# Performance work log

Measured on AMD Instinct MI355X. Metric: run time of the kernel, lower is better.

The kernel has to match this reference:

```python
import jax, jax.numpy as jnp
import numpy as np

N_NODES = 100000


def _gcn_layer(x, src, dst, W, b, num_nodes):
    # Linear transform first (PyG GCNConv applies Linear before propagate).
    h = x @ W.T  # [N, out]
    # Degree (with self loops already included in src/dst), computed on target.
    ones = jnp.ones(dst.shape[0], dtype=h.dtype)
    deg = jax.ops.segment_sum(ones, dst, num_segments=num_nodes)
    dinv = jnp.where(deg > 0, jax.lax.rsqrt(deg), 0.0)
    norm = dinv[src] * dinv[dst]  # [E]
    msg = h[src] * norm[:, None]  # gather + per-edge scale, [E, out]
    out = jax.ops.segment_sum(msg, dst, num_segments=num_nodes)
    return out + b


def setup_inputs() -> dict:
    key = jax.random.key(0)
    k1, k2, k3, k4, k5, k6 = jax.random.split(key, 6)
    d = 64
    x = jax.random.normal(k1, (N_NODES, d), dtype=jnp.float32)
    edge_index = jax.random.randint(k2, (2, 1600000), 0, N_NODES, dtype=jnp.int64)
    s = 1.0 / np.sqrt(d)
    W1 = jax.random.normal(k3, (d, d), dtype=jnp.float32) * s
    b1 = jax.random.normal(k4, (d,), dtype=jnp.float32) * 0.01
    W2 = jax.random.normal(k5, (d, d), dtype=jnp.float32) * s
    b2 = jax.random.normal(k6, (d,), dtype=jnp.float32) * 0.01
    return {"x": x, "edge_index": edge_index, "W1": W1, "b1": b1, "W2": W2, "b2": b2}


def reference(x, edge_index, W1, b1, W2, b2):
    n = x.shape[0]
    loop = jnp.arange(n, dtype=edge_index.dtype)
    src = jnp.concatenate([edge_index[0], loop])  # add self loops
    dst = jnp.concatenate([edge_index[1], loop])
    h = _gcn_layer(x, src, dst, W1, b1, n)
    out = _gcn_layer(h, src, dst, W2, b2, n)
    return out
```

## Files before the change

kernel.cpp:

```cpp
#include <hip/hip_runtime.h>
#include <hip/hip_fp16.h>


#define D 64
#define NPB 128
#define MAXB 784
#define CHUNK 8192

__global__ __launch_bounds__(256) void hist_kernel(const int* __restrict__ dst,
                                                   int* __restrict__ counts,
                                                   int nE, int B) {
    __shared__ int hist[MAXB];
    int c = blockIdx.x;
    for (int b = threadIdx.x; b < B; b += 256) hist[b] = 0;
    __syncthreads();
    int e0 = c * CHUNK;
#pragma unroll
    for (int i = 0; i < CHUNK / 256; ++i) {
        int e = e0 + i * 256 + threadIdx.x;
        if (e < nE) atomicAdd(&hist[dst[e] >> 7], 1);
    }
    __syncthreads();
    for (int b = threadIdx.x; b < B; b += 256) counts[c * B + b] = hist[b];
}

__global__ __launch_bounds__(256) void scan_chunks(const int* __restrict__ counts,
                                                   int* __restrict__ base,
                                                   int* __restrict__ bucketTotal,
                                                   int B, int C) {
    int b = blockIdx.x * 4 + (threadIdx.x >> 6);
    if (b >= B) return;
    int lane = threadIdx.x & 63;
    int running = 0;
    for (int c0 = 0; c0 < C; c0 += 64) {
        int c = c0 + lane;
        int v = (c < C) ? counts[c * B + b] : 0;
        int x = v;
#pragma unroll
        for (int s = 1; s < 64; s <<= 1) {
            int u = __shfl_up(x, s);
            if (lane >= s) x += u;
        }
        if (c < C) base[c * B + b] = running + x - v;
        running += __shfl(x, 63);
    }
    if (lane == 0) bucketTotal[b] = running;
}

__global__ __launch_bounds__(1024) void scan_buckets(const int* __restrict__ bucketTotal,
                                                     int* __restrict__ bucketBase, int B) {
    __shared__ int sdata[1024];
    int t = threadIdx.x;
    int v = (t < B) ? bucketTotal[t] : 0;
    sdata[t] = v;
    __syncthreads();
    for (int s = 1; s < 1024; s <<= 1) {
        int u = (t >= s) ? sdata[t - s] : 0;
        __syncthreads();
        sdata[t] += u;
        __syncthreads();
    }
    if (t < B) bucketBase[t] = sdata[t] - v;
    if (t == B - 1) bucketBase[B] = sdata[t];
}

__global__ __launch_bounds__(256) void scatter0_kernel(const int* __restrict__ src,
                                                       const int* __restrict__ dst,
                                                       const int* __restrict__ base,
                                                       const int* __restrict__ bbase,
                                                       int* __restrict__ entries0,
                                                       int nE, int B) {
    __shared__ int cur[MAXB];
    int c = blockIdx.x;
    for (int b = threadIdx.x; b < B; b += 256) cur[b] = base[c * B + b] + bbase[b];
    __syncthreads();
    int e0 = c * CHUNK;
#pragma unroll
    for (int i = 0; i < CHUNK / 256; ++i) {
        int e = e0 + i * 256 + threadIdx.x;
        if (e < nE) {
            int s = src[e], d = dst[e];
            int pos = atomicAdd(&cur[d >> 7], 1);
            entries0[pos] = s | ((d & (NPB - 1)) << 17);
        }
    }
}

__global__ __launch_bounds__(256) void regroup_count(const int* __restrict__ entries0,
                                                     const int* __restrict__ bbase,
                                                     int* __restrict__ off,
                                                     int* __restrict__ deg,
                                                     float* __restrict__ dinv, int N) {
    __shared__ int cnt[NPB];
    __shared__ int scn[NPB];
    int b = blockIdx.x;
    int t = threadIdx.x;
    if (t < NPB) cnt[t] = 0;
    __syncthreads();
    int s0 = bbase[b], s1 = bbase[b + 1];
    for (int p = s0 + t; p < s1; p += 256)
        atomicAdd(&cnt[(entries0[p] >> 17) & (NPB - 1)], 1);
    __syncthreads();
    if (t < NPB) scn[t] = cnt[t];
    __syncthreads();
    for (int s = 1; s < NPB; s <<= 1) {
        int u = 0;
        if (t < NPB && t >= s) u = scn[t - s];
        __syncthreads();
        if (t < NPB) scn[t] += u;
        __syncthreads();
    }
    if (t < NPB) {
        int node = b * NPB + t;
        if (node < N) {
            int c = cnt[t];
            off[node]  = s0 + scn[t] - c;
            deg[node]  = c;
            dinv[node] = rsqrtf((float)c + 1.0f);
        }
    }
}

__global__ __launch_bounds__(256) void regroup_scatter(const int* __restrict__ entries0,
                                                       const int* __restrict__ bbase,
                                                       const int* __restrict__ off,
                                                       const float* __restrict__ dinv,
                                                       int2* __restrict__ entries1, int N) {
    __shared__ int cur[NPB];
    int b = blockIdx.x;
    int t = threadIdx.x;
    if (t < NPB) {
        int node = b * NPB + t;
        cur[t] = (node < N) ? off[node] : 0;
    }
    __syncthreads();
    int s0 = bbase[b], s1 = bbase[b + 1];
    for (int p = s0 + t; p < s1; p += 256) {
        int e = entries0[p];
        int s = e & 0x1FFFF;
        int dloc = (e >> 17) & (NPB - 1);
        int pos = atomicAdd(&cur[dloc], 1);
        float nrm = dinv[s] * dinv[b * NPB + dloc];
        entries1[pos] = make_int2(s, __float_as_int(nrm));
    }
}

__global__ __launch_bounds__(256) void aggregate2(const int2* __restrict__ csr,
                                                  const int* __restrict__ off,
                                                  const int* __restrict__ deg,
                                                  const float* __restrict__ dinv,
                                                  const __half* __restrict__ H,
                                                  const float* __restrict__ bias,
                                                  float* __restrict__ out, int N) {
    int node = blockIdx.x * 4 + (threadIdx.x >> 6);
    if (node >= N) return;
    int lane = threadIdx.x & 63;
    int p2 = lane & 31;
    int h  = lane >> 5;
    const __half2* H2 = (const __half2*)H;
    float2 acc = make_float2(0.0f, 0.0f);
    int beg = off[node];
    int end = beg + deg[node];
    int p = beg;
    for (; p + 8 <= end; p += 8) {
        int2 e0 = csr[p + 0 + h];
        int2 e1 = csr[p + 2 + h];
        int2 e2 = csr[p + 4 + h];
        int2 e3 = csr[p + 6 + h];
        __half2 g0 = H2[(size_t)e0.x * 32 + p2];
        __half2 g1 = H2[(size_t)e1.x * 32 + p2];
        __half2 g2 = H2[(size_t)e2.x * 32 + p2];
        __half2 g3 = H2[(size_t)e3.x * 32 + p2];
        float c0 = __int_as_float(e0.y), c1 = __int_as_float(e1.y);
        float c2 = __int_as_float(e2.y), c3 = __int_as_float(e3.y);
        float2 f0 = __half22float2(g0), f1 = __half22float2(g1);
        float2 f2 = __half22float2(g2), f3 = __half22float2(g3);
        acc.x += f0.x * c0; acc.y += f0.y * c0;
        acc.x += f1.x * c1; acc.y += f1.y * c1;
        acc.x += f2.x * c2; acc.y += f2.y * c2;
        acc.x += f3.x * c3; acc.y += f3.y * c3;
    }
    for (; p + 2 <= end; p += 2) {
        int2 e0 = csr[p + h];
        __half2 g0 = H2[(size_t)e0.x * 32 + p2];
        float c0 = __int_as_float(e0.y);
        float2 f0 = __half22float2(g0);
        acc.x += f0.x * c0; acc.y += f0.y * c0;
    }
    if (p < end && h == 0) {
        int2 e0 = csr[p];
        __half2 g0 = H2[(size_t)e0.x * 32 + p2];
        float c0 = __int_as_float(e0.y);
        float2 f0 = __half22float2(g0);
        acc.x += f0.x * c0; acc.y += f0.y * c0;
    }
    acc.x += __shfl_xor(acc.x, 32);
    acc.y += __shfl_xor(acc.y, 32);
    if (h == 0) {
        float dd = dinv[node];
        float s = dd * dd;
        float2 hs = __half22float2(H2[(size_t)node * 32 + p2]);
        float2 bv = ((const float2*)bias)[p2];
        float2 o;
        o.x = acc.x + bv.x + hs.x * s;
        o.y = acc.y + bv.y + hs.y * s;
        ((float2*)(out + (size_t)node * D))[p2] = o;
    }
}

__global__ __launch_bounds__(256) void gemm_xwt_h(const float* __restrict__ X,
                                                  const float* __restrict__ W,
                                                  __half* __restrict__ H, int N) {
    __shared__ float xt[64 * 68];
    __shared__ float wt[64 * 68];
    const int t = threadIdx.x;
    const int i0 = blockIdx.x * 64;
#pragma unroll
    for (int r = 0; r < 16; ++r) {
        int idx = r * 256 + t;
        int j = idx >> 6, k = idx & 63;
        wt[k * 68 + j] = W[idx];
    }
#pragma unroll
    for (int r = 0; r < 16; ++r) {
        int idx = r * 256 + t;
        int i = idx >> 6, k = idx & 63;
        float v = 0.0f;
        if (i0 + i < N) v = X[(size_t)(i0 + i) * D + k];
        xt[k * 68 + i] = v;
    }
    __syncthreads();
    const int tn = (t & 15) * 4;
    const int tc = (t >> 4) * 4;
    float acc[4][4] = {};
#pragma unroll 8
    for (int k = 0; k < 64; ++k) {
        const float4 xa = *(const float4*)(xt + k * 68 + tn);
        const float4 wb = *(const float4*)(wt + k * 68 + tc);
        acc[0][0] += xa.x * wb.x; acc[0][1] += xa.x * wb.y; acc[0][2] += xa.x * wb.z; acc[0][3] += xa.x * wb.w;
        acc[1][0] += xa.y * wb.x; acc[1][1] += xa.y * wb.y; acc[1][2] += xa.y * wb.z; acc[1][3] += xa.y * wb.w;
        acc[2][0] += xa.z * wb.x; acc[2][1] += xa.z * wb.y; acc[2][2] += xa.z * wb.z; acc[2][3] += xa.z * wb.w;
        acc[3][0] += xa.w * wb.x; acc[3][1] += xa.w * wb.y; acc[3][2] += xa.w * wb.z; acc[3][3] += xa.w * wb.w;
    }
#pragma unroll
    for (int a = 0; a < 4; ++a) {
        int i = i0 + tn + a;
        if (i < N) {
            union { __half2 h2[2]; uint2 u2; } pk;
            pk.h2[0].x = __float2half_rn(acc[a][0]);
            pk.h2[0].y = __float2half_rn(acc[a][1]);
            pk.h2[1].x = __float2half_rn(acc[a][2]);
            pk.h2[1].y = __float2half_rn(acc[a][3]);
            *(uint2*)(&H[(size_t)i * D + tc]) = pk.u2;
        }
    }
}

__global__ __launch_bounds__(256) void deg_kernel(const int* __restrict__ dst,
                                                  int* __restrict__ deg, int nE) {
    int e = blockIdx.x * 256 + threadIdx.x;
    if (e < nE) atomicAdd(&deg[dst[e]], 1);
}

__global__ __launch_bounds__(256) void dinv_kernel(const int* __restrict__ deg,
                                                   float* __restrict__ dinv, int N) {
    int i = blockIdx.x * 256 + threadIdx.x;
    if (i < N) dinv[i] = rsqrtf((float)deg[i] + 1.0f);
}

__global__ __launch_bounds__(256) void gemm_xwt(const float* __restrict__ X,
                                                const float* __restrict__ W,
                                                float* __restrict__ H, int N) {
    __shared__ float xt[64 * 68];
    __shared__ float wt[64 * 68];
    const int t = threadIdx.x;
    const int i0 = blockIdx.x * 64;
#pragma unroll
    for (int r = 0; r < 16; ++r) {
        int idx = r * 256 + t;
        int j = idx >> 6, k = idx & 63;
        wt[k * 68 + j] = W[idx];
    }
#pragma unroll
    for (int r = 0; r < 16; ++r) {
        int idx = r * 256 + t;
        int i = idx >> 6, k = idx & 63;
        float v = 0.0f;
        if (i0 + i < N) v = X[(size_t)(i0 + i) * D + k];
        xt[k * 68 + i] = v;
    }
    __syncthreads();
    const int tn = (t & 15) * 4;
    const int tc = (t >> 4) * 4;
    float acc[4][4] = {};
#pragma unroll 8
    for (int k = 0; k < 64; ++k) {
        const float4 xa = *(const float4*)(xt + k * 68 + tn);
        const float4 wb = *(const float4*)(wt + k * 68 + tc);
        acc[0][0] += xa.x * wb.x; acc[0][1] += xa.x * wb.y; acc[0][2] += xa.x * wb.z; acc[0][3] += xa.x * wb.w;
        acc[1][0] += xa.y * wb.x; acc[1][1] += xa.y * wb.y; acc[1][2] += xa.y * wb.z; acc[1][3] += xa.y * wb.w;
        acc[2][0] += xa.z * wb.x; acc[2][1] += xa.z * wb.y; acc[2][2] += xa.z * wb.z; acc[2][3] += xa.z * wb.w;
        acc[3][0] += xa.w * wb.x; acc[3][1] += xa.w * wb.y; acc[3][2] += xa.w * wb.z; acc[3][3] += xa.w * wb.w;
    }
#pragma unroll
    for (int a = 0; a < 4; ++a) {
        int i = i0 + tn + a;
        if (i < N) {
            float4 o = make_float4(acc[a][0], acc[a][1], acc[a][2], acc[a][3]);
            *(float4*)(H + (size_t)i * D + tc) = o;
        }
    }
}

__global__ __launch_bounds__(256) void init_out(const float* __restrict__ H,
                                                const float* __restrict__ dinv,
                                                const float* __restrict__ b,
                                                float* __restrict__ out, int N) {
    int idx4 = blockIdx.x * 256 + threadIdx.x;
    if (idx4 >= N * 16) return;
    int i = idx4 >> 4;
    int jc = idx4 & 15;
    float di = dinv[i];
    float s = di * di;
    float4 h4 = ((const float4*)H)[idx4];
    float4 b4 = ((const float4*)b)[jc];
    ((float4*)out)[idx4] = make_float4(b4.x + h4.x * s, b4.y + h4.y * s,
                                       b4.z + h4.z * s, b4.w + h4.w * s);
}

__global__ __launch_bounds__(256) void edge_scatter(const int* __restrict__ src,
                                                    const int* __restrict__ dst,
                                                    const float* __restrict__ dinv,
                                                    const float* __restrict__ H,
                                                    float* __restrict__ out, int nE) {
    int tid = blockIdx.x * 256 + threadIdx.x;
    int e = tid >> 4;
    if (e >= nE) return;
    int l = tid & 15;
    int s = src[e];
    int d = dst[e];
    float c = dinv[s] * dinv[d];
    float4 v = ((const float4*)H)[s * 16 + l];
    float* o = out + (size_t)d * D + l * 4;
    unsafeAtomicAdd(o + 0, v.x * c);
    unsafeAtomicAdd(o + 1, v.y * c);
    unsafeAtomicAdd(o + 2, v.z * c);
    unsafeAtomicAdd(o + 3, v.w * c);
}

static inline size_t align_up(size_t v, size_t a) { return (v + a - 1) & ~(a - 1); }

extern "C" void kernel_launch(void* const* d_in, const int* in_sizes, int n_in,
                              void* d_out, int out_size, void* d_ws, size_t ws_size,
                              hipStream_t stream) {
    const float* x  = (const float*)d_in[0];
    const int*   ei = (const int*)d_in[1];
    const float* W1 = (const float*)d_in[2];
    const float* b1 = (const float*)d_in[3];
    const float* W2 = (const float*)d_in[4];
    const float* b2 = (const float*)d_in[5];
    float* out = (float*)d_out;

    const int N  = in_sizes[0] / D;
    const int nE = in_sizes[1] / 2;
    const int* src = ei;
    const int* dstv = ei + nE;

    const int B = (N + NPB - 1) / NPB;
    const int C = (nE + CHUNK - 1) / CHUNK;

    char* base_p = (char*)d_ws;
    size_t o = 0;
    int* counts = (int*)(base_p + o);  o = align_up(o + (size_t)C * B * 4, 256);
    int* cbase  = (int*)(base_p + o);  o = align_up(o + (size_t)C * B * 4, 256);
    int* btot   = (int*)(base_p + o);  o = align_up(o + (size_t)B * 4, 256);
    int* bbase  = (int*)(base_p + o);  o = align_up(o + (size_t)(B + 1) * 4, 256);
    int* off    = (int*)(base_p + o);  o = align_up(o + (size_t)N * 4, 256);
    int* deg    = (int*)(base_p + o);  o = align_up(o + (size_t)N * 4, 256);
    float* dinv = (float*)(base_p + o); o = align_up(o + (size_t)N * 4, 256);
    int2* entries1 = (int2*)(base_p + o); o = align_up(o + (size_t)nE * 8, 256);
    size_t r2 = (size_t)nE * 4 > (size_t)N * D * 2 ? (size_t)nE * 4 : (size_t)N * D * 2;
    int* entries0 = (int*)(base_p + o);
    __half* Hh    = (__half*)(base_p + o);
    o = align_up(o + r2, 256);
    size_t need = o;

    int gb_n = (N + 255) / 256;
    int gb_g = (N + 63) / 64;
    int gb_e = (nE + 255) / 256;

    if (ws_size >= need && B <= MAXB && B <= 1024) {
        hist_kernel<<<C, 256, 0, stream>>>(dstv, counts, nE, B);
        scan_chunks<<<(B + 3) / 4, 256, 0, stream>>>(counts, cbase, btot, B, C);
        scan_buckets<<<1, 1024, 0, stream>>>(btot, bbase, B);
        scatter0_kernel<<<C, 256, 0, stream>>>(src, dstv, cbase, bbase, entries0, nE, B);
        regroup_count<<<B, 256, 0, stream>>>(entries0, bbase, off, deg, dinv, N);
        regroup_scatter<<<B, 256, 0, stream>>>(entries0, bbase, off, dinv, entries1, N);

        int gb_a = (N + 3) / 4;
        gemm_xwt_h<<<gb_g, 256, 0, stream>>>(x, W1, Hh, N);
        aggregate2<<<gb_a, 256, 0, stream>>>(entries1, off, deg, dinv, Hh, b1, out, N);
        gemm_xwt_h<<<gb_g, 256, 0, stream>>>(out, W2, Hh, N);
        aggregate2<<<gb_a, 256, 0, stream>>>(entries1, off, deg, dinv, Hh, b2, out, N);
    } else {
        size_t fo = 0;
        int* fdeg    = (int*)(base_p + fo);  fo = align_up(fo + (size_t)N * 4, 256);
        float* fdinv = (float*)(base_p + fo); fo = align_up(fo + (size_t)N * 4, 256);
        float* bufA  = (float*)(base_p + fo);
        hipMemsetAsync(fdeg, 0, (size_t)N * 4, stream);
        deg_kernel<<<gb_e, 256, 0, stream>>>(dstv, fdeg, nE);
        dinv_kernel<<<gb_n, 256, 0, stream>>>(fdeg, fdinv, N);
        int gb_i = (N * 16 + 255) / 256;
        int gb_e16 = (int)(((long long)nE * 16 + 255) / 256);
        gemm_xwt<<<gb_g, 256, 0, stream>>>(x, W1, bufA, N);
        init_out<<<gb_i, 256, 0, stream>>>(bufA, fdinv, b1, out, N);
        edge_scatter<<<gb_e16, 256, 0, stream>>>(src, dstv, fdinv, bufA, out, nE);
        gemm_xwt<<<gb_g, 256, 0, stream>>>(out, W2, bufA, N);
        init_out<<<gb_i, 256, 0, stream>>>(bufA, fdinv, b2, out, N);
        edge_scatter<<<gb_e16, 256, 0, stream>>>(src, dstv, fdinv, bufA, out, nE);
    }
}
```

Measured before the change: 298.3 us.

## Fuse CSR build into one cooperative kernel, store layer-1 output in fp16

Replaces the six CSR-construction launches with a single cooperative kernel that uses grid-wide syncs between phases, falling back to the old launches if the cooperative launch fails. The chunk-scan results now overwrite the counts buffer in place. The first aggregation writes a half-precision intermediate that the second GEMM reads, and the aggregation loop gains a 16-edge unrolled path for more gathers in flight. The aims are to cut launch overhead and intermediate traffic, at the cost of fewer blocks per phase in the cooperative kernel and extra fp16 rounding of layer-1 activations.

```diff
diff --git a/kernel.cpp b/kernel.cpp
--- a/kernel.cpp
+++ b/kernel.cpp
@@ -1,11 +1,155 @@
 #include <hip/hip_runtime.h>
 #include <hip/hip_fp16.h>
+#include <hip/hip_cooperative_groups.h>
+#include <type_traits>
+
+namespace cg = cooperative_groups;
 
 
 #define D 64
 #define NPB 128
 #define MAXB 784
 #define CHUNK 8192
+
+__global__ __launch_bounds__(256) void build_coop2(const int* __restrict__ src,
+                                                   const int* __restrict__ dst,
+                                                   int* __restrict__ counts,
+                                                   int* __restrict__ btot,
+                                                   int* __restrict__ bbase,
+                                                   int* __restrict__ off,
+                                                   int* __restrict__ deg,
+                                                   float* __restrict__ dinv,
+                                                   int* __restrict__ entries0,
+                                                   int2* __restrict__ entries1,
+                                                   int nE, int B, int C, int N) {
+    cg::grid_group grid = cg::this_grid();
+    __shared__ int sm[MAXB];
+    const int t = threadIdx.x;
+
+    for (int c = blockIdx.x; c < C; c += gridDim.x) {
+        for (int b = t; b < B; b += 256) sm[b] = 0;
+        __syncthreads();
+        int e0 = c * CHUNK;
+#pragma unroll
+        for (int i = 0; i < CHUNK / 256; ++i) {
+            int e = e0 + i * 256 + t;
+            if (e < nE) atomicAdd(&sm[dst[e] >> 7], 1);
+        }
+        __syncthreads();
+        for (int b = t; b < B; b += 256) counts[c * B + b] = sm[b];
+        __syncthreads();
+    }
+    grid.sync();
+
+    for (int b = blockIdx.x * 4 + (t >> 6); b < B; b += gridDim.x * 4) {
+        int lane = t & 63;
+        int running = 0;
+        for (int c0 = 0; c0 < C; c0 += 64) {
+            int c = c0 + lane;
+            int v = (c < C) ? counts[c * B + b] : 0;
+            int x = v;
+#pragma unroll
+            for (int s = 1; s < 64; s <<= 1) {
+                int u = __shfl_up(x, s);
+                if (lane >= s) x += u;
+            }
+            if (c < C) counts[c * B + b] = running + x - v;
+            running += __shfl(x, 63);
+        }
+        if (lane == 0) btot[b] = running;
+    }
+    grid.sync();
+
+    if (blockIdx.x == 0) {
+        int i0 = t * 4;
+        int a0 = (i0 + 0 < B) ? btot[i0 + 0] : 0;
+        int a1 = (i0 + 1 < B) ? btot[i0 + 1] : 0;
+        int a2 = (i0 + 2 < B) ? btot[i0 + 2] : 0;
+        int a3 = (i0 + 3 < B) ? btot[i0 + 3] : 0;
+        int l0 = a0, l1 = l0 + a1, l2 = l1 + a2, l3 = l2 + a3;
+        sm[t] = l3;
+        __syncthreads();
+        for (int s = 1; s < 256; s <<= 1) {
+            int u = (t >= s) ? sm[t - s] : 0;
+            __syncthreads();
+            sm[t] += u;
+            __syncthreads();
+        }
+        int prefix = (t > 0) ? sm[t - 1] : 0;
+        if (i0 + 0 < B) bbase[i0 + 0] = prefix;
+        if (i0 + 1 < B) bbase[i0 + 1] = prefix + l0;
+        if (i0 + 2 < B) bbase[i0 + 2] = prefix + l1;
+        if (i0 + 3 < B) bbase[i0 + 3] = prefix + l2;
+        if (t == 255) bbase[B] = sm[255];
+    }
+    grid.sync();
+
+    for (int c = blockIdx.x; c < C; c += gridDim.x) {
+        for (int b = t; b < B; b += 256) sm[b] = counts[c * B + b] + bbase[b];
+        __syncthreads();
+        int e0 = c * CHUNK;
+#pragma unroll
+        for (int i = 0; i < CHUNK / 256; ++i) {
+            int e = e0 + i * 256 + t;
+            if (e < nE) {
+                int s = src[e], d = dst[e];
+                int pos = atomicAdd(&sm[d >> 7], 1);
+                entries0[pos] = s | ((d & (NPB - 1)) << 17);
+            }
+        }
+        __syncthreads();
+    }
+    grid.sync();
+
+    for (int b = blockIdx.x; b < B; b += gridDim.x) {
+        int* cnt = sm;
+        int* scn = sm + NPB;
+        if (t < NPB) cnt[t] = 0;
+        __syncthreads();
+        int s0 = bbase[b], s1 = bbase[b + 1];
+        for (int p = s0 + t; p < s1; p += 256)
+            atomicAdd(&cnt[(entries0[p] >> 17) & (NPB - 1)], 1);
+        __syncthreads();
+        if (t < NPB) scn[t] = cnt[t];
+        __syncthreads();
+        for (int s = 1; s < NPB; s <<= 1) {
+            int u = 0;
+            if (t < NPB && t >= s) u = scn[t - s];
+            __syncthreads();
+            if (t < NPB) scn[t] += u;
+            __syncthreads();
+        }
+        if (t < NPB) {
+            int node = b * NPB + t;
+            if (node < N) {
+                int c = cnt[t];
+                off[node]  = s0 + scn[t] - c;
+                deg[node]  = c;
+                dinv[node] = rsqrtf((float)c + 1.0f);
+            }
+        }
+        __syncthreads();
+    }
+    grid.sync();
+
+    for (int b = blockIdx.x; b < B; b += gridDim.x) {
+        if (t < NPB) {
+            int node = b * NPB + t;
+            sm[t] = (node < N) ? off[node] : 0;
+        }
+        __syncthreads();
+        int s0 = bbase[b], s1 = bbase[b + 1];
+        for (int p = s0 + t; p < s1; p += 256) {
+            int e = entries0[p];
+            int s = e & 0x1FFFF;
+            int dloc = (e >> 17) & (NPB - 1);
+            int pos = atomicAdd(&sm[dloc], 1);
+            float nrm = dinv[s] * dinv[b * NPB + dloc];
+            entries1[pos] = make_int2(s, __float_as_int(nrm));
+        }
+        __syncthreads();
+    }
+}
 
 __global__ __launch_bounds__(256) void hist_kernel(const int* __restrict__ dst,
                                                    int* __restrict__ counts,
@@ -24,8 +168,7 @@
     for (int b = threadIdx.x; b < B; b += 256) counts[c * B + b] = hist[b];
 }
 
-__global__ __launch_bounds__(256) void scan_chunks(const int* __restrict__ counts,
-                                                   int* __restrict__ base,
+__global__ __launch_bounds__(256) void scan_chunks(int* __restrict__ counts,
                                                    int* __restrict__ bucketTotal,
                                                    int B, int C) {
     int b = blockIdx.x * 4 + (threadIdx.x >> 6);
@@ -41,7 +184,7 @@
             int u = __shfl_up(x, s);
             if (lane >= s) x += u;
         }
-        if (c < C) base[c * B + b] = running + x - v;
+        if (c < C) counts[c * B + b] = running + x - v;
         running += __shfl(x, 63);
     }
     if (lane == 0) bucketTotal[b] = running;
@@ -145,13 +288,14 @@
     }
 }
 
+template <typename OutT>
 __global__ __launch_bounds__(256) void aggregate2(const int2* __restrict__ csr,
                                                   const int* __restrict__ off,
                                                   const int* __restrict__ deg,
                                                   const float* __restrict__ dinv,
                                                   const __half* __restrict__ H,
                                                   const float* __restrict__ bias,
-                                                  float* __restrict__ out, int N) {
+                                                  OutT* __restrict__ out, int N) {
     int node = blockIdx.x * 4 + (threadIdx.x >> 6);
     if (node >= N) return;
     int lane = threadIdx.x & 63;
@@ -162,36 +306,46 @@
     int beg = off[node];
     int end = beg + deg[node];
     int p = beg;
+    for (; p + 16 <= end; p += 16) {
+        int2 e[8];
+#pragma unroll
+        for (int i = 0; i < 8; ++i) e[i] = csr[p + 2 * i + h];
+        __half2 g[8];
+#pragma unroll
+        for (int i = 0; i < 8; ++i) g[i] = H2[(size_t)e[i].x * 32 + p2];
+#pragma unroll
+        for (int i = 0; i < 8; ++i) {
+            float2 f = __half22float2(g[i]);
+            float c = __int_as_float(e[i].y);
+            acc.x += f.x * c; acc.y += f.y * c;
+        }
+    }
     for (; p + 8 <= end; p += 8) {
-        int2 e0 = csr[p + 0 + h];
-        int2 e1 = csr[p + 2 + h];
-        int2 e2 = csr[p + 4 + h];
-        int2 e3 = csr[p + 6 + h];
+        int2 e0 = csr[p + 0 + h], e1 = csr[p + 2 + h];
+        int2 e2 = csr[p + 4 + h], e3 = csr[p + 6 + h];
         __half2 g0 = H2[(size_t)e0.x * 32 + p2];
         __half2 g1 = H2[(size_t)e1.x * 32 + p2];
         __half2 g2 = H2[(size_t)e2.x * 32 + p2];
         __half2 g3 = H2[(size_t)e3.x * 32 + p2];
-        float c0 = __int_as_float(e0.y), c1 = __int_as_float(e1.y);
-        float c2 = __int_as_float(e2.y), c3 = __int_as_float(e3.y);
         float2 f0 = __half22float2(g0), f1 = __half22float2(g1);
         float2 f2 = __half22float2(g2), f3 = __half22float2(g3);
-        acc.x += f0.x * c0; acc.y += f0.y * c0;
-        acc.x += f1.x * c1; acc.y += f1.y * c1;
-        acc.x += f2.x * c2; acc.y += f2.y * c2;
-        acc.x += f3.x * c3; acc.y += f3.y * c3;
+        acc.x += f0.x * __int_as_float(e0.y); acc.y += f0.y * __int_as_float(e0.y);
+        acc.x += f1.x * __int_as_float(e1.y); acc.y += f1.y * __int_as_float(e1.y);
+        acc.x += f2.x * __int_as_float(e2.y); acc.y += f2.y * __int_as_float(e2.y);
+        acc.x += f3.x * __int_as_float(e3.y); acc.y += f3.y * __int_as_float(e3.y);
     }
     for (; p + 2 <= end; p += 2) {
         int2 e0 = csr[p + h];
         __half2 g0 = H2[(size_t)e0.x * 32 + p2];
+        float2 f0 = __half22float2(g0);
         float c0 = __int_as_float(e0.y);
-        float2 f0 = __half22float2(g0);
         acc.x += f0.x * c0; acc.y += f0.y * c0;
     }
     if (p < end && h == 0) {
         int2 e0 = csr[p];
         __half2 g0 = H2[(size_t)e0.x * 32 + p2];
+        float2 f0 = __half22float2(g0);
         float c0 = __int_as_float(e0.y);
-        float2 f0 = __half22float2(g0);
         acc.x += f0.x * c0; acc.y += f0.y * c0;
     }
     acc.x += __shfl_xor(acc.x, 32);
@@ -204,11 +358,16 @@
         float2 o;
         o.x = acc.x + bv.x + hs.x * s;
         o.y = acc.y + bv.y + hs.y * s;
-        ((float2*)(out + (size_t)node * D))[p2] = o;
-    }
-}
-
-__global__ __launch_bounds__(256) void gemm_xwt_h(const float* __restrict__ X,
+        if constexpr (sizeof(OutT) == 2) {
+            ((__half2*)(out + (size_t)node * D))[p2] = __float22half2_rn(o);
+        } else {
+            ((float2*)(out + (size_t)node * D))[p2] = o;
+        }
+    }
+}
+
+template <typename InT>
+__global__ __launch_bounds__(256) void gemm_xwt_h(const InT* __restrict__ X,
                                                   const float* __restrict__ W,
                                                   __half* __restrict__ H, int N) {
     __shared__ float xt[64 * 68];
@@ -226,7 +385,12 @@
         int idx = r * 256 + t;
         int i = idx >> 6, k = idx & 63;
         float v = 0.0f;
-        if (i0 + i < N) v = X[(size_t)(i0 + i) * D + k];
+        if (i0 + i < N) {
+            if constexpr (sizeof(InT) == 2)
+                v = __half2float(((const __half*)X)[(size_t)(i0 + i) * D + k]);
+            else
+                v = ((const float*)X)[(size_t)(i0 + i) * D + k];
+        }
         xt[k * 68 + i] = v;
     }
     __syncthreads();
@@ -363,7 +527,7 @@
 
     const int N  = in_sizes[0] / D;
     const int nE = in_sizes[1] / 2;
-    const int* src = ei;
+    const int* srcp = ei;
     const int* dstv = ei + nE;
 
     const int B = (N + NPB - 1) / NPB;
@@ -372,7 +536,6 @@
     char* base_p = (char*)d_ws;
     size_t o = 0;
     int* counts = (int*)(base_p + o);  o = align_up(o + (size_t)C * B * 4, 256);
-    int* cbase  = (int*)(base_p + o);  o = align_up(o + (size_t)C * B * 4, 256);
     int* btot   = (int*)(base_p + o);  o = align_up(o + (size_t)B * 4, 256);
     int* bbase  = (int*)(base_p + o);  o = align_up(o + (size_t)(B + 1) * 4, 256);
     int* off    = (int*)(base_p + o);  o = align_up(o + (size_t)N * 4, 256);
@@ -383,25 +546,45 @@
     int* entries0 = (int*)(base_p + o);
     __half* Hh    = (__half*)(base_p + o);
     o = align_up(o + r2, 256);
-    size_t need = o;
+    size_t need_base = o;
+    __half* A1h = (__half*)(base_p + o);
+    size_t need_full = o + align_up((size_t)N * D * 2, 256);
 
     int gb_n = (N + 255) / 256;
     int gb_g = (N + 63) / 64;
     int gb_e = (nE + 255) / 256;
 
-    if (ws_size >= need && B <= MAXB && B <= 1024) {
-        hist_kernel<<<C, 256, 0, stream>>>(dstv, counts, nE, B);
-        scan_chunks<<<(B + 3) / 4, 256, 0, stream>>>(counts, cbase, btot, B, C);
-        scan_buckets<<<1, 1024, 0, stream>>>(btot, bbase, B);
-        scatter0_kernel<<<C, 256, 0, stream>>>(src, dstv, cbase, bbase, entries0, nE, B);
-        regroup_count<<<B, 256, 0, stream>>>(entries0, bbase, off, deg, dinv, N);
-        regroup_scatter<<<B, 256, 0, stream>>>(entries0, bbase, off, dinv, entries1, N);
+    if (ws_size >= need_base && B <= MAXB && B <= 1024) {
+        int GB = B;
+        int nE_ = nE, B_ = B, C_ = C, N_ = N;
+        const int* src_ = srcp; const int* dst_ = dstv;
+        int* counts_ = counts; int* btot_ = btot; int* bbase_ = bbase;
+        int* off_ = off; int* deg_ = deg; float* dinv_ = dinv;
+        int* e0_ = entries0; int2* e1_ = entries1;
+        void* kargs[] = {&src_, &dst_, &counts_, &btot_, &bbase_, &off_, &deg_,
+                         &dinv_, &e0_, &e1_, &nE_, &B_, &C_, &N_};
+        hipError_t cerr = hipLaunchCooperativeKernel((const void*)build_coop2,
+                                                     dim3(GB), dim3(256),
+                                                     kargs, 0, stream);
+        if (cerr != hipSuccess) {
+            hist_kernel<<<C, 256, 0, stream>>>(dstv, counts, nE, B);
+            scan_chunks<<<(B + 3) / 4, 256, 0, stream>>>(counts, btot, B, C);
+            scan_buckets<<<1, 1024, 0, stream>>>(btot, bbase, B);
+            scatter0_kernel<<<C, 256, 0, stream>>>(srcp, dstv, counts, bbase, entries0, nE, B);
+            regroup_count<<<B, 256, 0, stream>>>(entries0, bbase, off, deg, dinv, N);
+            regroup_scatter<<<B, 256, 0, stream>>>(entries0, bbase, off, dinv, entries1, N);
+        }
 
         int gb_a = (N + 3) / 4;
-        gemm_xwt_h<<<gb_g, 256, 0, stream>>>(x, W1, Hh, N);
-        aggregate2<<<gb_a, 256, 0, stream>>>(entries1, off, deg, dinv, Hh, b1, out, N);
-        gemm_xwt_h<<<gb_g, 256, 0, stream>>>(out, W2, Hh, N);
-        aggregate2<<<gb_a, 256, 0, stream>>>(entries1, off, deg, dinv, Hh, b2, out, N);
+        gemm_xwt_h<float><<<gb_g, 256, 0, stream>>>(x, W1, Hh, N);
+        if (ws_size >= need_full) {
+            aggregate2<__half><<<gb_a, 256, 0, stream>>>(entries1, off, deg, dinv, Hh, b1, A1h, N);
+            gemm_xwt_h<__half><<<gb_g, 256, 0, stream>>>(A1h, W2, Hh, N);
+        } else {
+            aggregate2<float><<<gb_a, 256, 0, stream>>>(entries1, off, deg, dinv, Hh, b1, out, N);
+            gemm_xwt_h<float><<<gb_g, 256, 0, stream>>>(out, W2, Hh, N);
+        }
+        aggregate2<float><<<gb_a, 256, 0, stream>>>(entries1, off, deg, dinv, Hh, b2, out, N);
     } else {
         size_t fo = 0;
         int* fdeg    = (int*)(base_p + fo);  fo = align_up(fo + (size_t)N * 4, 256);
@@ -414,9 +597,9 @@
         int gb_e16 = (int)(((long long)nE * 16 + 255) / 256);
         gemm_xwt<<<gb_g, 256, 0, stream>>>(x, W1, bufA, N);
         init_out<<<gb_i, 256, 0, stream>>>(bufA, fdinv, b1, out, N);
-        edge_scatter<<<gb_e16, 256, 0, stream>>>(src, dstv, fdinv, bufA, out, nE);
+        edge_scatter<<<gb_e16, 256, 0, stream>>>(srcp, dstv, fdinv, bufA, out, nE);
         gemm_xwt<<<gb_g, 256, 0, stream>>>(out, W2, bufA, N);
         init_out<<<gb_i, 256, 0, stream>>>(bufA, fdinv, b2, out, N);
-        edge_scatter<<<gb_e16, 256, 0, stream>>>(src, dstv, fdinv, bufA, out, nE);
-    }
-}
+        edge_scatter<<<gb_e16, 256, 0, stream>>>(srcp, dstv, fdinv, bufA, out, nE);
+    }
+}
```

After: 716.0 us. 140% more time.

## Store layer-1 output in fp16, unroll aggregation deeper, scan counts in place

Applied to the files above, without the earlier changes.

The layer-1 aggregation now writes its output in half precision to a separate workspace buffer, and the second GEMM reads it as fp16, halving that intermediate's traffic. The aggregation loop gains a 16-edge unrolled body with eight gathers in flight per lane. The chunk scan now writes its prefixes back into the counts array instead of a separate buffer, and the bucket scan uses 256 threads that each handle four elements. Rounding the intermediate to fp16 adds precision loss, and the deeper unroll may raise register pressure.

```diff
diff --git a/kernel.cpp b/kernel.cpp
--- a/kernel.cpp
+++ b/kernel.cpp
@@ -24,8 +24,7 @@
     for (int b = threadIdx.x; b < B; b += 256) counts[c * B + b] = hist[b];
 }
 
-__global__ __launch_bounds__(256) void scan_chunks(const int* __restrict__ counts,
-                                                   int* __restrict__ base,
+__global__ __launch_bounds__(256) void scan_chunks(int* __restrict__ counts,
                                                    int* __restrict__ bucketTotal,
                                                    int B, int C) {
     int b = blockIdx.x * 4 + (threadIdx.x >> 6);
@@ -41,27 +40,36 @@
             int u = __shfl_up(x, s);
             if (lane >= s) x += u;
         }
-        if (c < C) base[c * B + b] = running + x - v;
+        if (c < C) counts[c * B + b] = running + x - v;
         running += __shfl(x, 63);
     }
     if (lane == 0) bucketTotal[b] = running;
 }
 
-__global__ __launch_bounds__(1024) void scan_buckets(const int* __restrict__ bucketTotal,
-                                                     int* __restrict__ bucketBase, int B) {
-    __shared__ int sdata[1024];
+__global__ __launch_bounds__(256) void scan_buckets(const int* __restrict__ btot,
+                                                    int* __restrict__ bbase, int B) {
+    __shared__ int sm[256];
     int t = threadIdx.x;
-    int v = (t < B) ? bucketTotal[t] : 0;
-    sdata[t] = v;
-    __syncthreads();
-    for (int s = 1; s < 1024; s <<= 1) {
-        int u = (t >= s) ? sdata[t - s] : 0;
+    int i0 = t * 4;
+    int a0 = (i0 + 0 < B) ? btot[i0 + 0] : 0;
+    int a1 = (i0 + 1 < B) ? btot[i0 + 1] : 0;
+    int a2 = (i0 + 2 < B) ? btot[i0 + 2] : 0;
+    int a3 = (i0 + 3 < B) ? btot[i0 + 3] : 0;
+    int l0 = a0, l1 = l0 + a1, l2 = l1 + a2, l3 = l2 + a3;
+    sm[t] = l3;
+    __syncthreads();
+    for (int s = 1; s < 256; s <<= 1) {
+        int u = (t >= s) ? sm[t - s] : 0;
         __syncthreads();
-        sdata[t] += u;
+        sm[t] += u;
         __syncthreads();
     }
-    if (t < B) bucketBase[t] = sdata[t] - v;
-    if (t == B - 1) bucketBase[B] = sdata[t];
+    int prefix = (t > 0) ? sm[t - 1] : 0;
+    if (i0 + 0 < B) bbase[i0 + 0] = prefix;
+    if (i0 + 1 < B) bbase[i0 + 1] = prefix + l0;
+    if (i0 + 2 < B) bbase[i0 + 2] = prefix + l1;
+    if (i0 + 3 < B) bbase[i0 + 3] = prefix + l2;
+    if (t == 255) bbase[B] = sm[255];
 }
 
 __global__ __launch_bounds__(256) void scatter0_kernel(const int* __restrict__ src,
@@ -145,13 +153,14 @@
     }
 }
 
+template <typename OutT>
 __global__ __launch_bounds__(256) void aggregate2(const int2* __restrict__ csr,
                                                   const int* __restrict__ off,
                                                   const int* __restrict__ deg,
                                                   const float* __restrict__ dinv,
                                                   const __half* __restrict__ H,
                                                   const float* __restrict__ bias,
-                                                  float* __restrict__ out, int N) {
+                                                  OutT* __restrict__ out, int N) {
     int node = blockIdx.x * 4 + (threadIdx.x >> 6);
     if (node >= N) return;
     int lane = threadIdx.x & 63;
@@ -162,36 +171,46 @@
     int beg = off[node];
     int end = beg + deg[node];
     int p = beg;
+    for (; p + 16 <= end; p += 16) {
+        int2 e[8];
+#pragma unroll
+        for (int i = 0; i < 8; ++i) e[i] = csr[p + 2 * i + h];
+        __half2 g[8];
+#pragma unroll
+        for (int i = 0; i < 8; ++i) g[i] = H2[(size_t)e[i].x * 32 + p2];
+#pragma unroll
+        for (int i = 0; i < 8; ++i) {
+            float2 f = __half22float2(g[i]);
+            float c = __int_as_float(e[i].y);
+            acc.x += f.x * c; acc.y += f.y * c;
+        }
+    }
     for (; p + 8 <= end; p += 8) {
-        int2 e0 = csr[p + 0 + h];
-        int2 e1 = csr[p + 2 + h];
-        int2 e2 = csr[p + 4 + h];
-        int2 e3 = csr[p + 6 + h];
+        int2 e0 = csr[p + 0 + h], e1 = csr[p + 2 + h];
+        int2 e2 = csr[p + 4 + h], e3 = csr[p + 6 + h];
         __half2 g0 = H2[(size_t)e0.x * 32 + p2];
         __half2 g1 = H2[(size_t)e1.x * 32 + p2];
         __half2 g2 = H2[(size_t)e2.x * 32 + p2];
         __half2 g3 = H2[(size_t)e3.x * 32 + p2];
-        float c0 = __int_as_float(e0.y), c1 = __int_as_float(e1.y);
-        float c2 = __int_as_float(e2.y), c3 = __int_as_float(e3.y);
         float2 f0 = __half22float2(g0), f1 = __half22float2(g1);
         float2 f2 = __half22float2(g2), f3 = __half22float2(g3);
-        acc.x += f0.x * c0; acc.y += f0.y * c0;
-        acc.x += f1.x * c1; acc.y += f1.y * c1;
-        acc.x += f2.x * c2; acc.y += f2.y * c2;
-        acc.x += f3.x * c3; acc.y += f3.y * c3;
+        acc.x += f0.x * __int_as_float(e0.y); acc.y += f0.y * __int_as_float(e0.y);
+        acc.x += f1.x * __int_as_float(e1.y); acc.y += f1.y * __int_as_float(e1.y);
+        acc.x += f2.x * __int_as_float(e2.y); acc.y += f2.y * __int_as_float(e2.y);
+        acc.x += f3.x * __int_as_float(e3.y); acc.y += f3.y * __int_as_float(e3.y);
     }
     for (; p + 2 <= end; p += 2) {
         int2 e0 = csr[p + h];
         __half2 g0 = H2[(size_t)e0.x * 32 + p2];
+        float2 f0 = __half22float2(g0);
         float c0 = __int_as_float(e0.y);
-        float2 f0 = __half22float2(g0);
         acc.x += f0.x * c0; acc.y += f0.y * c0;
     }
     if (p < end && h == 0) {
         int2 e0 = csr[p];
         __half2 g0 = H2[(size_t)e0.x * 32 + p2];
+        float2 f0 = __half22float2(g0);
         float c0 = __int_as_float(e0.y);
-        float2 f0 = __half22float2(g0);
         acc.x += f0.x * c0; acc.y += f0.y * c0;
     }
     acc.x += __shfl_xor(acc.x, 32);
@@ -204,11 +223,16 @@
         float2 o;
         o.x = acc.x + bv.x + hs.x * s;
         o.y = acc.y + bv.y + hs.y * s;
-        ((float2*)(out + (size_t)node * D))[p2] = o;
-    }
-}
-
-__global__ __launch_bounds__(256) void gemm_xwt_h(const float* __restrict__ X,
+        if constexpr (sizeof(OutT) == 2) {
+            ((__half2*)(out + (size_t)node * D))[p2] = __float22half2_rn(o);
+        } else {
+            ((float2*)(out + (size_t)node * D))[p2] = o;
+        }
+    }
+}
+
+template <typename InT>
+__global__ __launch_bounds__(256) void gemm_xwt_h(const InT* __restrict__ X,
                                                   const float* __restrict__ W,
                                                   __half* __restrict__ H, int N) {
     __shared__ float xt[64 * 68];
@@ -226,7 +250,12 @@
         int idx = r * 256 + t;
         int i = idx >> 6, k = idx & 63;
         float v = 0.0f;
-        if (i0 + i < N) v = X[(size_t)(i0 + i) * D + k];
+        if (i0 + i < N) {
+            if constexpr (sizeof(InT) == 2)
+                v = __half2float(((const __half*)X)[(size_t)(i0 + i) * D + k]);
+            else
+                v = ((const float*)X)[(size_t)(i0 + i) * D + k];
+        }
         xt[k * 68 + i] = v;
     }
     __syncthreads();
@@ -363,7 +392,7 @@
 
     const int N  = in_sizes[0] / D;
     const int nE = in_sizes[1] / 2;
-    const int* src = ei;
+    const int* srcp = ei;
     const int* dstv = ei + nE;
 
     const int B = (N + NPB - 1) / NPB;
@@ -372,7 +401,6 @@
     char* base_p = (char*)d_ws;
     size_t o = 0;
     int* counts = (int*)(base_p + o);  o = align_up(o + (size_t)C * B * 4, 256);
-    int* cbase  = (int*)(base_p + o);  o = align_up(o + (size_t)C * B * 4, 256);
     int* btot   = (int*)(base_p + o);  o = align_up(o + (size_t)B * 4, 256);
     int* bbase  = (int*)(base_p + o);  o = align_up(o + (size_t)(B + 1) * 4, 256);
     int* off    = (int*)(base_p + o);  o = align_up(o + (size_t)N * 4, 256);
@@ -383,25 +411,32 @@
     int* entries0 = (int*)(base_p + o);
     __half* Hh    = (__half*)(base_p + o);
     o = align_up(o + r2, 256);
-    size_t need = o;
+    size_t need_base = o;
+    __half* A1h = (__half*)(base_p + o);
+    size_t need_full = o + align_up((size_t)N * D * 2, 256);
 
     int gb_n = (N + 255) / 256;
     int gb_g = (N + 63) / 64;
     int gb_e = (nE + 255) / 256;
 
-    if (ws_size >= need && B <= MAXB && B <= 1024) {
+    if (ws_size >= need_base && B <= MAXB && B <= 1024) {
         hist_kernel<<<C, 256, 0, stream>>>(dstv, counts, nE, B);
-        scan_chunks<<<(B + 3) / 4, 256, 0, stream>>>(counts, cbase, btot, B, C);
-        scan_buckets<<<1, 1024, 0, stream>>>(btot, bbase, B);
-        scatter0_kernel<<<C, 256, 0, stream>>>(src, dstv, cbase, bbase, entries0, nE, B);
+        scan_chunks<<<(B + 3) / 4, 256, 0, stream>>>(counts, btot, B, C);
+        scan_buckets<<<1, 256, 0, stream>>>(btot, bbase, B);
+        scatter0_kernel<<<C, 256, 0, stream>>>(srcp, dstv, counts, bbase, entries0, nE, B);
         regroup_count<<<B, 256, 0, stream>>>(entries0, bbase, off, deg, dinv, N);
         regroup_scatter<<<B, 256, 0, stream>>>(entries0, bbase, off, dinv, entries1, N);
 
         int gb_a = (N + 3) / 4;
-        gemm_xwt_h<<<gb_g, 256, 0, stream>>>(x, W1, Hh, N);
-        aggregate2<<<gb_a, 256, 0, stream>>>(entries1, off, deg, dinv, Hh, b1, out, N);
-        gemm_xwt_h<<<gb_g, 256, 0, stream>>>(out, W2, Hh, N);
-        aggregate2<<<gb_a, 256, 0, stream>>>(entries1, off, deg, dinv, Hh, b2, out, N);
+        gemm_xwt_h<float><<<gb_g, 256, 0, stream>>>(x, W1, Hh, N);
+        if (ws_size >= need_full) {
+            aggregate2<__half><<<gb_a, 256, 0, stream>>>(entries1, off, deg, dinv, Hh, b1, A1h, N);
+            gemm_xwt_h<__half><<<gb_g, 256, 0, stream>>>(A1h, W2, Hh, N);
+        } else {
+            aggregate2<float><<<gb_a, 256, 0, stream>>>(entries1, off, deg, dinv, Hh, b1, out, N);
+            gemm_xwt_h<float><<<gb_g, 256, 0, stream>>>(out, W2, Hh, N);
+        }
+        aggregate2<float><<<gb_a, 256, 0, stream>>>(entries1, off, deg, dinv, Hh, b2, out, N);
     } else {
         size_t fo = 0;
         int* fdeg    = (int*)(base_p + fo);  fo = align_up(fo + (size_t)N * 4, 256);
@@ -414,9 +449,9 @@
         int gb_e16 = (int)(((long long)nE * 16 + 255) / 256);
         gemm_xwt<<<gb_g, 256, 0, stream>>>(x, W1, bufA, N);
         init_out<<<gb_i, 256, 0, stream>>>(bufA, fdinv, b1, out, N);
-        edge_scatter<<<gb_e16, 256, 0, stream>>>(src, dstv, fdinv, bufA, out, nE);
+        edge_scatter<<<gb_e16, 256, 0, stream>>>(srcp, dstv, fdinv, bufA, out, nE);
         gemm_xwt<<<gb_g, 256, 0, stream>>>(out, W2, bufA, N);
         init_out<<<gb_i, 256, 0, stream>>>(bufA, fdinv, b2, out, N);
-        edge_scatter<<<gb_e16, 256, 0, stream>>>(src, dstv, fdinv, bufA, out, nE);
-    }
-}
+        edge_scatter<<<gb_e16, 256, 0, stream>>>(srcp, dstv, fdinv, bufA, out, nE);
+    }
+}
```

After: 299.9 us. No clear change (+0.5%).
